# Optimization experiments

Hardware: AMD Instinct MI355X
Metric: run time of the kernel (lower is better)

The kernel has to match this reference:

```python
import jax, jax.numpy as jnp
import numpy as np

N_NODES = 100000


def _gcn_conv(x, W, b, src, dst, n):
    # PyG GCNConv: add self-loops, sym-normalize by deg^{-1/2}, then X W + b
    h = x @ W  # [N, out]
    ones = jnp.ones(src.shape[0], dtype=x.dtype)
    deg = jax.ops.segment_sum(ones, dst, num_segments=n) + 1.0  # +1 for self loop
    dinv = jax.lax.rsqrt(deg)
    norm = dinv[src] * dinv[dst]  # [E]
    agg = jax.ops.segment_sum(h[src] * norm[:, None], dst, num_segments=n)
    agg = agg + h * (dinv * dinv)[:, None]  # self-loop contribution
    return agg + b


def setup_inputs() -> dict:
    key = jax.random.key(0)
    k1, k2, k3, k4 = jax.random.split(key, 4)
    n, e = N_NODES, 1600000
    in_d, hid_d, out_d = 128, 128, 64
    x = jax.random.normal(k1, (n, in_d), dtype=jnp.float32)
    edge_index = jax.random.randint(k2, (2, e), 0, n, dtype=jnp.int64)
    s1 = 1.0 / np.sqrt(in_d)
    s2 = 1.0 / np.sqrt(hid_d)
    W1 = jax.random.uniform(k3, (in_d, hid_d), jnp.float32, -s1, s1)
    W2 = jax.random.uniform(k4, (hid_d, out_d), jnp.float32, -s2, s2)
    b1 = jnp.zeros((hid_d,), jnp.float32)
    b2 = jnp.zeros((out_d,), jnp.float32)
    return {"x": x, "edge_index": edge_index, "W1": W1, "b1": b1, "W2": W2, "b2": b2}


def reference(x, edge_index, W1, b1, W2, b2):
    src, dst = edge_index[0], edge_index[1]
    n = x.shape[0]
    h = _gcn_conv(x, W1, b1, src, dst, n)
    h = jax.nn.relu(h)
    # dropout p=0.2 is identity at eval time
    out = _gcn_conv(h, W2, b2, src, dst, n)
    return out
```

## Files before the change

### kernel.cpp

```cpp
#include <hip/hip_runtime.h>


typedef unsigned int u32;
using bfrag = __attribute__((ext_vector_type(8))) short;
using f4    = __attribute__((ext_vector_type(4))) float;

__device__ inline u32 pack_bf16(float a, float b) {
    u32 ua = __float_as_uint(a);
    u32 ub = __float_as_uint(b);
    ua += 0x7fffu + ((ua >> 16) & 1u);
    ub += 0x7fffu + ((ub >> 16) & 1u);
    return (ua >> 16) | (ub & 0xffff0000u);
}
__device__ inline float bf_lo(u32 v) { return __uint_as_float(v << 16); }
__device__ inline float bf_hi(u32 v) { return __uint_as_float(v & 0xffff0000u); }

__device__ inline u32 pack_w(float w) {
    u32 b = __float_as_uint(w) + 0x800u;
    if (b < 0x3B800000u) b = 0x3B800000u;
    if (b > 0x3F800000u) b = 0x3F800000u;
    return (b - 0x3B800000u) >> 12;
}
__device__ inline float dec_w(u32 e) {
    return __uint_as_float(((e & 0x7fffu) << 12) + 0x3B800000u);
}

__device__ inline bfrag as_bfrag(uint4 v) {
    union { uint4 u; bfrag b; } x; x.u = v; return x.b;
}

__device__ inline void prep_w_chunk(int idx, const float* __restrict__ W1,
                                    const float* __restrict__ W2,
                                    u32* __restrict__ W1t, u32* __restrict__ W2t) {
    if (idx < 128 * 64) {
        int nr = idx >> 6, kd = idx & 63;
        W1t[idx] = pack_bf16(W1[(2 * kd) * 128 + nr], W1[(2 * kd + 1) * 128 + nr]);
    } else if (idx < 128 * 64 + 64 * 64) {
        int i = idx - 128 * 64;
        int nr = i >> 6, kd = i & 63;
        W2t[i] = pack_bf16(W2[(2 * kd) * 64 + nr], W2[(2 * kd + 1) * 64 + nr]);
    }
}


template <int OUT, bool ABF>
__device__ inline void gemm_body(int bid, const void* __restrict__ Ap,
                                 const u32* __restrict__ Wt,
                                 u32* __restrict__ C, int n) {
    constexpr int NT = OUT / 16;
    const int lane = threadIdx.x & 63;
    const int wv   = threadIdx.x >> 6;
    const int r15  = lane & 15;
    const int quad = lane >> 4;
    const int rowbase = bid * 128 + wv * 32;

    bfrag af[2][4];
#pragma unroll
    for (int mi = 0; mi < 2; ++mi) {
        int row = rowbase + mi * 16 + r15;
        row = (row < n) ? row : (n - 1);
        if constexpr (ABF) {
            const u32* ar = (const u32*)Ap + (size_t)row * 64 + quad * 4;
#pragma unroll
            for (int ks = 0; ks < 4; ++ks)
                af[mi][ks] = as_bfrag(*(const uint4*)(ar + ks * 16));
        } else {
            const float* arf = (const float*)Ap + (size_t)row * 128 + quad * 8;
#pragma unroll
            for (int ks = 0; ks < 4; ++ks) {
                float4 v0 = *(const float4*)(arf + ks * 32);
                float4 v1 = *(const float4*)(arf + ks * 32 + 4);
                uint4 p;
                p.x = pack_bf16(v0.x, v0.y);
                p.y = pack_bf16(v0.z, v0.w);
                p.z = pack_bf16(v1.x, v1.y);
                p.w = pack_bf16(v1.z, v1.w);
                af[mi][ks] = as_bfrag(p);
            }
        }
    }

    f4 acc[2][NT];
#pragma unroll
    for (int mi = 0; mi < 2; ++mi)
#pragma unroll
        for (int nt = 0; nt < NT; ++nt) acc[mi][nt] = (f4)0.0f;

#pragma unroll
    for (int nt = 0; nt < NT; ++nt) {
        const u32* wr = Wt + (size_t)(nt * 16 + r15) * 64 + quad * 4;
#pragma unroll
        for (int ks = 0; ks < 4; ++ks) {
            bfrag bf = as_bfrag(*(const uint4*)(wr + ks * 16));
            acc[0][nt] = __builtin_amdgcn_mfma_f32_16x16x32_bf16(bf, af[0][ks], acc[0][nt], 0, 0, 0);
            acc[1][nt] = __builtin_amdgcn_mfma_f32_16x16x32_bf16(bf, af[1][ks], acc[1][nt], 0, 0, 0);
        }
    }

#pragma unroll
    for (int mi = 0; mi < 2; ++mi) {
        int row = rowbase + mi * 16 + r15;
        if (row < n) {
            u32* cp = C + (size_t)row * (OUT / 2);
#pragma unroll
            for (int nt = 0; nt < NT; ++nt) {
                uint2 p;
                p.x = pack_bf16(acc[mi][nt][0], acc[mi][nt][1]);
                p.y = pack_bf16(acc[mi][nt][2], acc[mi][nt][3]);
                *(uint2*)(cp + nt * 8 + quad * 2) = p;
            }
        }
    }
}


__global__ __launch_bounds__(256) void count_bins_pw(const int* __restrict__ dst,
                                                     int* __restrict__ bc,
                                                     int E, int nbin, int nb3, int M,
                                                     const float* __restrict__ W1,
                                                     const float* __restrict__ W2,
                                                     u32* __restrict__ W1t,
                                                     u32* __restrict__ W2t) {
    __shared__ int hist[512];
    if (blockIdx.x >= (unsigned)nb3) {
        prep_w_chunk((blockIdx.x - nb3) * 256 + threadIdx.x, W1, W2, W1t, W2t);
        return;
    }
    if (blockIdx.x == 0 && threadIdx.x == 0) bc[M] = E;
    for (int t = threadIdx.x; t < nbin; t += 256) hist[t] = 0;
    __syncthreads();
    const int base = blockIdx.x * 2048 + threadIdx.x;
#pragma unroll
    for (int k = 0; k < 8; ++k) {
        int e = base + k * 256;
        if (e < E) atomicAdd(&hist[dst[e] >> 8], 1);
    }
    __syncthreads();
    for (int t = threadIdx.x; t < nbin; t += 256)
        bc[(size_t)t * nb3 + blockIdx.x] = hist[t];
}

__global__ __launch_bounds__(1024) void scan_reduce_g(const int* __restrict__ a,
                                                      int* __restrict__ bsum, int M) {
    __shared__ int wsum[16];
    int i = blockIdx.x * 1024 + threadIdx.x;
    int v = (i < M) ? a[i] : 0;
#pragma unroll
    for (int off = 32; off > 0; off >>= 1) v += __shfl_down(v, off);
    const int lane = threadIdx.x & 63;
    const int wid  = threadIdx.x >> 6;
    if (lane == 0) wsum[wid] = v;
    __syncthreads();
    if (threadIdx.x < 16) {
        int s = wsum[threadIdx.x];
#pragma unroll
        for (int off = 8; off > 0; off >>= 1) s += __shfl_down(s, off);
        if (threadIdx.x == 0) bsum[blockIdx.x] = s;
    }
}

__global__ __launch_bounds__(1024) void scan_apply_g2(int* __restrict__ a,
                                                      const int* __restrict__ bsum,
                                                      int nb, int M) {
    __shared__ int wsum[16];
    __shared__ int base_s;
    const int lane = threadIdx.x & 63;
    const int wid  = threadIdx.x >> 6;
    int pv = 0;
    for (int t = threadIdx.x; t < (int)blockIdx.x; t += 1024) pv += bsum[t];
#pragma unroll
    for (int off = 32; off > 0; off >>= 1) pv += __shfl_down(pv, off);
    if (lane == 0) wsum[wid] = pv;
    __syncthreads();
    if (threadIdx.x == 0) {
        int s = 0;
#pragma unroll
        for (int w = 0; w < 16; ++w) s += wsum[w];
        base_s = s;
    }
    __syncthreads();
    const int boff = base_s;
    int i = blockIdx.x * 1024 + threadIdx.x;
    int v = (i < M) ? a[i] : 0;
    int x = v;
#pragma unroll
    for (int off = 1; off < 64; off <<= 1) {
        int t = __shfl_up(x, off);
        if (lane >= off) x += t;
    }
    if (lane == 63) wsum[wid] = x;
    __syncthreads();
    if (wid == 0 && lane < 16) {
        int w = wsum[lane];
#pragma unroll
        for (int off = 1; off < 16; off <<= 1) {
            int t = __shfl_up(w, off);
            if (lane >= off) w += t;
        }
        wsum[lane] = w;
    }
    __syncthreads();
    int wave_excl = (wid == 0) ? 0 : wsum[wid - 1];
    if (i < M) a[i] = boff + wave_excl + (x - v);
}

__global__ __launch_bounds__(256) void scatter_bins(const int* __restrict__ src,
                                                    const int* __restrict__ dst,
                                                    const int* __restrict__ offs,
                                                    u32* __restrict__ tmp,
                                                    int E, int nbin, int nb3) {
    __shared__ int cur[512];
    for (int t = threadIdx.x; t < nbin; t += 256)
        cur[t] = offs[(size_t)t * nb3 + blockIdx.x];
    __syncthreads();
    const int base = blockIdx.x * 2048 + threadIdx.x;
#pragma unroll
    for (int k = 0; k < 8; ++k) {
        int e = base + k * 256;
        if (e < E) {
            int d = dst[e];
            int pos = atomicAdd(&cur[d >> 8], 1);
            tmp[pos] = ((u32)(d & 255) << 17) | (u32)src[e];
        }
    }
}

__global__ __launch_bounds__(256) void bucket_hist(const u32* __restrict__ tmp,
                                                   const int* __restrict__ offs,
                                                   int* __restrict__ row_ptr,
                                                   float* __restrict__ dinv,
                                                   int n, int nb3, int E) {
    __shared__ int hist[256];
    __shared__ int wtot[4];
    const int b   = blockIdx.x;
    const int beg = offs[(size_t)b * nb3];
    const int end = offs[(size_t)(b + 1) * nb3];
    hist[threadIdx.x] = 0;
    __syncthreads();
    for (int i = beg + threadIdx.x; i < end; i += 256)
        atomicAdd(&hist[tmp[i] >> 17], 1);
    __syncthreads();
    const int lane = threadIdx.x & 63;
    const int wid  = threadIdx.x >> 6;
    int v = hist[threadIdx.x];
    int x = v;
#pragma unroll
    for (int off = 1; off < 64; off <<= 1) {
        int t = __shfl_up(x, off);
        if (lane >= off) x += t;
    }
    if (lane == 63) wtot[wid] = x;
    __syncthreads();
    int wbase = 0;
    for (int w = 0; w < wid; ++w) wbase += wtot[w];
    const int rp = beg + wbase + x - v;
    const int d = b * 256 + threadIdx.x;
    if (d < n) {
        row_ptr[d] = rp;
        dinv[d]    = rsqrtf((float)v + 1.0f);
    }
    if (b == 0 && threadIdx.x == 0) row_ptr[n] = E;
}

__global__ __launch_bounds__(256) void bucket_ew_gemm1(
    const u32* __restrict__ tmp, const int* __restrict__ offs,
    const int* __restrict__ row_ptr, const float* __restrict__ dinv,
    u32* __restrict__ ew, int n, int nb3, int nbin,
    const float* __restrict__ x, const u32* __restrict__ W1t,
    u32* __restrict__ h1u) {
    if (blockIdx.x >= (unsigned)nbin) {
        gemm_body<128, false>(blockIdx.x - nbin, x, W1t, h1u, n);
        return;
    }
    __shared__ int   cur[256];
    __shared__ float sdi[256];
    const int b = blockIdx.x;
    const int t = threadIdx.x;
    const int beg = offs[(size_t)b * nb3];
    const int end = offs[(size_t)(b + 1) * nb3];
    const int d = b * 256 + t;
    cur[t] = row_ptr[(d <= n) ? d : n];
    sdi[t] = (d < n) ? dinv[d] : 0.0f;
    __syncthreads();
    for (int i = beg + t; i < end; i += 256) {
        u32 r = tmp[i];
        int k = r >> 17;
        int pos = atomicAdd(&cur[k], 1);
        u32 s = r & 0x1ffffu;
        ew[pos] = (s << 15) | pack_w(dinv[s] * sdi[k]);
    }
}


template <int OUT, bool ABF>
__global__ __launch_bounds__(256) void gemm_mfma(const void* __restrict__ Ap,
                                                 const u32* __restrict__ Wt,
                                                 u32* __restrict__ C, int n) {
    gemm_body<OUT, ABF>(blockIdx.x, Ap, Wt, C, n);
}


__global__ __launch_bounds__(256) void gather128(const u32* __restrict__ h,
                                                 const float* __restrict__ dinv,
                                                 const int* __restrict__ row_ptr,
                                                 const u32* __restrict__ ew,
                                                 const float* __restrict__ bias,
                                                 u32* __restrict__ outp, int n) {
    const int lane = threadIdx.x & 63;
    int node = blockIdx.x * 4 + (threadIdx.x >> 6);
    if (node >= n) return;
    node = __builtin_amdgcn_readfirstlane(node);

    const float dd  = dinv[node];
    const int   beg = __builtin_amdgcn_readfirstlane(row_ptr[node]);
    const int   end = __builtin_amdgcn_readfirstlane(row_ptr[node + 1]);

    u32 sv = h[(size_t)node * 64 + lane];
    float2 b = ((const float2*)bias)[lane];
    float acc0 = fmaf(bf_lo(sv) * dd, dd, b.x);
    float acc1 = fmaf(bf_hi(sv) * dd, dd, b.y);

    int j = beg;
    for (; j + 16 <= end; j += 16) {
        u32 ep[16];
#pragma unroll
        for (int k = 0; k < 16; ++k) ep[k] = ew[j + k];
        u32 v[16];
#pragma unroll
        for (int k = 0; k < 16; ++k)
            v[k] = h[((size_t)(ep[k] >> 15) << 6) + lane];
#pragma unroll
        for (int k = 0; k < 16; ++k) {
            float wf = dec_w(ep[k]);
            acc0 = fmaf(wf, bf_lo(v[k]), acc0);
            acc1 = fmaf(wf, bf_hi(v[k]), acc1);
        }
    }
    for (; j < end; j += 8) {
        const int cnt = end - j;
        u32 ep[8];
#pragma unroll
        for (int k = 0; k < 8; ++k) {
            int c = j + k;
            ep[k] = ew[(c < end) ? c : end - 1];
        }
        u32 v[8];
#pragma unroll
        for (int k = 0; k < 8; ++k)
            v[k] = h[((size_t)(ep[k] >> 15) << 6) + lane];
#pragma unroll
        for (int k = 0; k < 8; ++k) {
            float wf = (k < cnt) ? dec_w(ep[k]) : 0.0f;
            acc0 = fmaf(wf, bf_lo(v[k]), acc0);
            acc1 = fmaf(wf, bf_hi(v[k]), acc1);
        }
    }

    outp[(size_t)node * 64 + lane] = pack_bf16(fmaxf(acc0, 0.0f), fmaxf(acc1, 0.0f));
}

__global__ __launch_bounds__(256) void gather64(const u32* __restrict__ h,
                                                const float* __restrict__ dinv,
                                                const int* __restrict__ row_ptr,
                                                const u32* __restrict__ ew,
                                                const float* __restrict__ bias,
                                                float* __restrict__ outp, int n) {
    const int lane   = threadIdx.x & 63;
    const int lane32 = lane & 31;
    const int sub    = lane >> 5;
    int node = blockIdx.x * 4 + (threadIdx.x >> 6);
    if (node >= n) return;
    node = __builtin_amdgcn_readfirstlane(node);

    const int beg = __builtin_amdgcn_readfirstlane(row_ptr[node]);
    const int end = __builtin_amdgcn_readfirstlane(row_ptr[node + 1]);

    float acc0 = 0.0f, acc1 = 0.0f;
    if (sub == 0) {
        const float dd = dinv[node];
        u32 sv = h[(size_t)node * 32 + lane32];
        float2 b = ((const float2*)bias)[lane32];
        acc0 = fmaf(bf_lo(sv) * dd, dd, b.x);
        acc1 = fmaf(bf_hi(sv) * dd, dd, b.y);
    }

    int j = beg;
    for (; j + 16 <= end; j += 16) {
        u32 ep[16];
#pragma unroll
        for (int k = 0; k < 16; ++k) ep[k] = ew[j + k];
        u32 v[8]; float wl[8];
#pragma unroll
        for (int p = 0; p < 8; ++p) {
            u32 e0 = ep[2 * p], e1 = ep[2 * p + 1];
            u32 so = sub ? (e1 >> 15) : (e0 >> 15);
            wl[p]  = sub ? dec_w(e1) : dec_w(e0);
            v[p]   = h[((size_t)so << 5) + lane32];
        }
#pragma unroll
        for (int p = 0; p < 8; ++p) {
            acc0 = fmaf(wl[p], bf_lo(v[p]), acc0);
            acc1 = fmaf(wl[p], bf_hi(v[p]), acc1);
        }
    }
    for (; j < end; j += 8) {
        const int cnt = end - j;
        u32 ep[8];
#pragma unroll
        for (int k = 0; k < 8; ++k) {
            int c = j + k;
            ep[k] = ew[(c < end) ? c : end - 1];
        }
        u32 v[4]; float wl[4];
#pragma unroll
        for (int p = 0; p < 4; ++p) {
            u32 e0 = ep[2 * p], e1 = ep[2 * p + 1];
            float w0 = (2 * p     < cnt) ? dec_w(e0) : 0.0f;
            float w1 = (2 * p + 1 < cnt) ? dec_w(e1) : 0.0f;
            u32 so = sub ? (e1 >> 15) : (e0 >> 15);
            wl[p]  = sub ? w1 : w0;
            v[p]   = h[((size_t)so << 5) + lane32];
        }
#pragma unroll
        for (int p = 0; p < 4; ++p) {
            acc0 = fmaf(wl[p], bf_lo(v[p]), acc0);
            acc1 = fmaf(wl[p], bf_hi(v[p]), acc1);
        }
    }

    acc0 += __shfl_xor(acc0, 32);
    acc1 += __shfl_xor(acc1, 32);
    if (sub == 0)
        ((float2*)(outp + (size_t)node * 64))[lane32] = make_float2(acc0, acc1);
}

extern "C" void kernel_launch(void* const* d_in, const int* in_sizes, int n_in,
                              void* d_out, int out_size, void* d_ws, size_t ws_size,
                              hipStream_t stream) {
    const float* x  = (const float*)d_in[0];
    const int*   ei = (const int*)d_in[1];
    const float* W1 = (const float*)d_in[2];
    const float* b1 = (const float*)d_in[3];
    const float* W2 = (const float*)d_in[4];
    const float* b2 = (const float*)d_in[5];
    float*       out = (float*)d_out;

    const int n = in_sizes[0] / 128;
    const int E = in_sizes[1] / 2;
    const int* srcv = ei;
    const int* dstv = ei + E;

    const int NP = 102400;
    u32* wsd = (u32*)d_ws;
    float* dinv    = (float*)wsd;
    int*   row_ptr = (int*)(wsd + NP);
    u32*   ew      = wsd + 2 * (size_t)NP;
    u32*   h1u     = ew + E;
    u32*   agg1b   = h1u + (size_t)n * 64;
    u32*   W1t     = agg1b + (size_t)n * 64;
    u32*   W2t     = W1t + 8192;
    u32*   h2u     = h1u;

    int*   bco  = (int*)agg1b;
    u32*   tmp2 = agg1b + 400000;
    int*   bsum = (int*)(agg1b + 2200000);

    const int NBIN = (n + 255) >> 8;
    const int NB3  = (E + 2047) / 2048;
    const int M    = NBIN * NB3;
    const int MB   = (M + 1023) / 1024;

    const int gblocks = (n + 127) / 128;

    count_bins_pw<<<NB3 + 48, 256, 0, stream>>>(dstv, bco, E, NBIN, NB3, M,
                                                W1, W2, W1t, W2t);
    scan_reduce_g<<<MB, 1024, 0, stream>>>(bco, bsum, M);
    scan_apply_g2<<<MB, 1024, 0, stream>>>(bco, bsum, MB, M);
    scatter_bins<<<NB3, 256, 0, stream>>>(srcv, dstv, bco, tmp2, E, NBIN, NB3);
    bucket_hist<<<NBIN, 256, 0, stream>>>(tmp2, bco, row_ptr, dinv, n, NB3, E);
    bucket_ew_gemm1<<<NBIN + gblocks, 256, 0, stream>>>(tmp2, bco, row_ptr, dinv,
                                                        ew, n, NB3, NBIN,
                                                        x, W1t, h1u);

    gather128<<<(n + 3) / 4, 256, 0, stream>>>(h1u, dinv, row_ptr, ew, b1, agg1b, n);

    gemm_mfma<64, true><<<gblocks, 256, 0, stream>>>(agg1b, W2t, h2u, n);
    gather64<<<(n + 3) / 4, 256, 0, stream>>>(h2u, dinv, row_ptr, ew, b2, out, n);
}
```

Baseline: 290.1 us.

## Fuse layer-1 gather with layer-2 GEMM via shared-memory tile

Merges the first-layer neighbor aggregation with the second-layer MFMA GEMM. Each block aggregates 32 nodes into shared memory as bf16 and then multiplies that tile by W2 directly. This removes the write and re-read of the intermediate aggregated activations and one kernel launch. In exchange each block is larger (32 nodes, 8 per wave processed serially) with a block-wide barrier, which may reduce latency hiding and load balance for the irregular gathers.

```diff
diff --git a/kernel.cpp b/kernel.cpp
--- a/kernel.cpp
+++ b/kernel.cpp
@@ -292,72 +292,102 @@
 }
 
 
-template <int OUT, bool ABF>
-__global__ __launch_bounds__(256) void gemm_mfma(const void* __restrict__ Ap,
-                                                 const u32* __restrict__ Wt,
-                                                 u32* __restrict__ C, int n) {
-    gemm_body<OUT, ABF>(blockIdx.x, Ap, Wt, C, n);
-}
-
-
-__global__ __launch_bounds__(256) void gather128(const u32* __restrict__ h,
-                                                 const float* __restrict__ dinv,
-                                                 const int* __restrict__ row_ptr,
-                                                 const u32* __restrict__ ew,
-                                                 const float* __restrict__ bias,
-                                                 u32* __restrict__ outp, int n) {
+__global__ __launch_bounds__(256) void gather128_gemm2(
+    const u32* __restrict__ h, const float* __restrict__ dinv,
+    const int* __restrict__ row_ptr, const u32* __restrict__ ew,
+    const float* __restrict__ bias, const u32* __restrict__ W2t,
+    u32* __restrict__ h2, int n) {
+    __shared__ u32 sh_a[32][68];
     const int lane = threadIdx.x & 63;
-    int node = blockIdx.x * 4 + (threadIdx.x >> 6);
-    if (node >= n) return;
-    node = __builtin_amdgcn_readfirstlane(node);
-
-    const float dd  = dinv[node];
-    const int   beg = __builtin_amdgcn_readfirstlane(row_ptr[node]);
-    const int   end = __builtin_amdgcn_readfirstlane(row_ptr[node + 1]);
-
-    u32 sv = h[(size_t)node * 64 + lane];
-    float2 b = ((const float2*)bias)[lane];
-    float acc0 = fmaf(bf_lo(sv) * dd, dd, b.x);
-    float acc1 = fmaf(bf_hi(sv) * dd, dd, b.y);
-
-    int j = beg;
-    for (; j + 16 <= end; j += 16) {
-        u32 ep[16];
-#pragma unroll
-        for (int k = 0; k < 16; ++k) ep[k] = ew[j + k];
-        u32 v[16];
-#pragma unroll
-        for (int k = 0; k < 16; ++k)
-            v[k] = h[((size_t)(ep[k] >> 15) << 6) + lane];
-#pragma unroll
-        for (int k = 0; k < 16; ++k) {
-            float wf = dec_w(ep[k]);
-            acc0 = fmaf(wf, bf_lo(v[k]), acc0);
-            acc1 = fmaf(wf, bf_hi(v[k]), acc1);
-        }
-    }
-    for (; j < end; j += 8) {
-        const int cnt = end - j;
-        u32 ep[8];
-#pragma unroll
-        for (int k = 0; k < 8; ++k) {
-            int c = j + k;
-            ep[k] = ew[(c < end) ? c : end - 1];
-        }
-        u32 v[8];
-#pragma unroll
-        for (int k = 0; k < 8; ++k)
-            v[k] = h[((size_t)(ep[k] >> 15) << 6) + lane];
-#pragma unroll
-        for (int k = 0; k < 8; ++k) {
-            float wf = (k < cnt) ? dec_w(ep[k]) : 0.0f;
-            acc0 = fmaf(wf, bf_lo(v[k]), acc0);
-            acc1 = fmaf(wf, bf_hi(v[k]), acc1);
-        }
-    }
-
-    outp[(size_t)node * 64 + lane] = pack_bf16(fmaxf(acc0, 0.0f), fmaxf(acc1, 0.0f));
-}
+    const int wv   = threadIdx.x >> 6;
+    const int tile0 = blockIdx.x * 32;
+
+    for (int ni = 0; ni < 8; ++ni) {
+        const int r = wv * 8 + ni;
+        int node = tile0 + r;
+        if (node < n) {
+            node = __builtin_amdgcn_readfirstlane(node);
+            const float dd  = dinv[node];
+            const int   beg = __builtin_amdgcn_readfirstlane(row_ptr[node]);
+            const int   end = __builtin_amdgcn_readfirstlane(row_ptr[node + 1]);
+
+            u32 sv = h[(size_t)node * 64 + lane];
+            float2 b = ((const float2*)bias)[lane];
+            float acc0 = fmaf(bf_lo(sv) * dd, dd, b.x);
+            float acc1 = fmaf(bf_hi(sv) * dd, dd, b.y);
+
+            int j = beg;
+            for (; j + 16 <= end; j += 16) {
+                u32 ep[16];
+#pragma unroll
+                for (int k = 0; k < 16; ++k) ep[k] = ew[j + k];
+                u32 v[16];
+#pragma unroll
+                for (int k = 0; k < 16; ++k)
+                    v[k] = h[((size_t)(ep[k] >> 15) << 6) + lane];
+#pragma unroll
+                for (int k = 0; k < 16; ++k) {
+                    float wf = dec_w(ep[k]);
+                    acc0 = fmaf(wf, bf_lo(v[k]), acc0);
+                    acc1 = fmaf(wf, bf_hi(v[k]), acc1);
+                }
+            }
+            for (; j < end; j += 8) {
+                const int cnt = end - j;
+                u32 ep[8];
+#pragma unroll
+                for (int k = 0; k < 8; ++k) {
+                    int c = j + k;
+                    ep[k] = ew[(c < end) ? c : end - 1];
+                }
+                u32 v[8];
+#pragma unroll
+                for (int k = 0; k < 8; ++k)
+                    v[k] = h[((size_t)(ep[k] >> 15) << 6) + lane];
+#pragma unroll
+                for (int k = 0; k < 8; ++k) {
+                    float wf = (k < cnt) ? dec_w(ep[k]) : 0.0f;
+                    acc0 = fmaf(wf, bf_lo(v[k]), acc0);
+                    acc1 = fmaf(wf, bf_hi(v[k]), acc1);
+                }
+            }
+            sh_a[r][lane] = pack_bf16(fmaxf(acc0, 0.0f), fmaxf(acc1, 0.0f));
+        }
+    }
+    __syncthreads();
+
+    const int r15  = lane & 15;
+    const int quad = lane >> 4;
+    bfrag af[2][4];
+#pragma unroll
+    for (int mi = 0; mi < 2; ++mi)
+#pragma unroll
+        for (int ks = 0; ks < 4; ++ks)
+            af[mi][ks] = as_bfrag(*(const uint4*)&sh_a[mi * 16 + r15][ks * 16 + quad * 4]);
+
+    f4 acc[2];
+    acc[0] = (f4)0.0f;
+    acc[1] = (f4)0.0f;
+    const u32* wr = W2t + (size_t)(wv * 16 + r15) * 64 + quad * 4;
+#pragma unroll
+    for (int ks = 0; ks < 4; ++ks) {
+        bfrag bf = as_bfrag(*(const uint4*)(wr + ks * 16));
+        acc[0] = __builtin_amdgcn_mfma_f32_16x16x32_bf16(bf, af[0][ks], acc[0], 0, 0, 0);
+        acc[1] = __builtin_amdgcn_mfma_f32_16x16x32_bf16(bf, af[1][ks], acc[1], 0, 0, 0);
+    }
+#pragma unroll
+    for (int mi = 0; mi < 2; ++mi) {
+        int row = tile0 + mi * 16 + r15;
+        if (row < n) {
+            u32* cp = h2 + (size_t)row * 32 + wv * 8 + quad * 2;
+            uint2 p;
+            p.x = pack_bf16(acc[mi][0], acc[mi][1]);
+            p.y = pack_bf16(acc[mi][2], acc[mi][3]);
+            *(uint2*)cp = p;
+        }
+    }
+}
+
 
 __global__ __launch_bounds__(256) void gather64(const u32* __restrict__ h,
                                                 const float* __restrict__ dinv,
@@ -456,14 +486,14 @@
     int*   row_ptr = (int*)(wsd + NP);
     u32*   ew      = wsd + 2 * (size_t)NP;
     u32*   h1u     = ew + E;
-    u32*   agg1b   = h1u + (size_t)n * 64;
-    u32*   W1t     = agg1b + (size_t)n * 64;
+    u32*   buf2    = h1u + (size_t)n * 64;
+    u32*   W1t     = buf2 + (size_t)n * 64;
     u32*   W2t     = W1t + 8192;
-    u32*   h2u     = h1u;
-
-    int*   bco  = (int*)agg1b;
-    u32*   tmp2 = agg1b + 400000;
-    int*   bsum = (int*)(agg1b + 2200000);
+    u32*   h2u     = buf2;
+
+    int*   bco  = (int*)buf2;
+    u32*   tmp2 = buf2 + 400000;
+    int*   bsum = (int*)(buf2 + 2200000);
 
     const int NBIN = (n + 255) >> 8;
     const int NB3  = (E + 2047) / 2048;
@@ -482,8 +512,8 @@
                                                         ew, n, NB3, NBIN,
                                                         x, W1t, h1u);
 
-    gather128<<<(n + 3) / 4, 256, 0, stream>>>(h1u, dinv, row_ptr, ew, b1, agg1b, n);
-
-    gemm_mfma<64, true><<<gblocks, 256, 0, stream>>>(agg1b, W2t, h2u, n);
+    gather128_gemm2<<<(n + 31) / 32, 256, 0, stream>>>(h1u, dinv, row_ptr, ew,
+                                                       b1, W2t, h2u, n);
+
     gather64<<<(n + 3) / 4, 256, 0, stream>>>(h2u, dinv, row_ptr, ew, b2, out, n);
 }
```

Result: faster. 283.3 us (-2.4%).
